# Optimization experiments

Measured on AMD Instinct MI355X. Metric: run time of the kernel, lower is better.

Reference implementation:

```python
import jax, jax.numpy as jnp
import numpy as np

EPS = 1e-5
NUM_SUBSET = 3

def conv1x1(x, w, b):
    # x: (N,C,T,V), w: (O,C), b: (O,)
    return jnp.einsum('nctv,oc->notv', x, w) + b[None, :, None, None]

def batchnorm(x, w, b):
    m = x.mean(axis=(0, 2, 3), keepdims=True)
    v = x.var(axis=(0, 2, 3), keepdims=True)
    return (x - m) * jax.lax.rsqrt(v + EPS) * w[None, :, None, None] + b[None, :, None, None]

def setup_inputs() -> dict:
    key = jax.random.key(0)
    ks = jax.random.split(key, 16)
    N, C, T, V, R, O, S = 32, 64, 256, 25, 8, 64, NUM_SUBSET
    sc = 0.05
    return {
        'x1': jax.random.normal(ks[0], (N, C, T, V), jnp.float32),
        'x2': jax.random.normal(ks[1], (N, C, T, V), jnp.float32),
        'PA': jax.random.normal(ks[2], (S, V, V), jnp.float32) * sc,
        'alpha': jnp.zeros((1,), jnp.float32),
        'c1w': jax.random.normal(ks[3], (S, R, C), jnp.float32) * sc,
        'c1b': jnp.zeros((S, R), jnp.float32),
        'c2w': jax.random.normal(ks[4], (S, R, C), jnp.float32) * sc,
        'c2b': jnp.zeros((S, R), jnp.float32),
        'c3w': jax.random.normal(ks[5], (S, O, C), jnp.float32) * sc,
        'c3b': jnp.zeros((S, O), jnp.float32),
        'c4w': jax.random.normal(ks[6], (S, O, C), jnp.float32) * sc,
        'c4b': jnp.zeros((S, O), jnp.float32),
        'c5w': jax.random.normal(ks[7], (S, O, R), jnp.float32) * sc,
        'c5b': jnp.zeros((S, O), jnp.float32),
        'c6w': jax.random.normal(ks[8], (S, O, R), jnp.float32) * sc,
        'c6b': jnp.zeros((S, O), jnp.float32),
        'bn1_w': jax.random.uniform(ks[9], (O,), jnp.float32),
        'bn1_b': jnp.zeros((O,), jnp.float32),
        'bn2_w': jax.random.uniform(ks[10], (O,), jnp.float32),
        'bn2_b': jnp.zeros((O,), jnp.float32),
    }

def reference(x1, x2, PA, alpha, c1w, c1b, c2w, c2b, c3w, c3b, c4w, c4b,
              c5w, c5b, c6w, c6b, bn1_w, bn1_b, bn2_w, bn2_b):
    y1 = y2 = None
    for i in range(NUM_SUBSET):
        r1 = conv1x1(x1, c1w[i], c1b[i]).mean(axis=2)  # (N,R,V)
        r2 = conv1x1(x2, c2w[i], c2b[i]).mean(axis=2)  # (N,R,V)
        x3 = conv1x1(x1, c3w[i], c3b[i])               # (N,O,T,V)
        x4 = conv1x1(x2, c4w[i], c4b[i])               # (N,O,T,V)
        rel = jnp.tanh(r1[:, :, :, None] - r2[:, :, None, :])  # (N,R,V,V)
        # NOTE: source passes self.alpha (scalar param) into the A2 slot,
        # so the `alpha` multiplier on conv5 defaults to 1.
        a1 = jnp.einsum('nruv,or->nouv', rel, c5w[i]) + c5b[i][None, :, None, None]
        a1 = a1 + PA[i][None, None, :, :]
        a2 = jnp.einsum('nruv,or->nouv', rel, c6w[i]) + c6b[i][None, :, None, None] + alpha
        z1 = jnp.einsum('ncuv,nctv->nctu', a1, x3)
        z2 = jnp.einsum('ncuv,nctv->nctu', a2, x4)
        y1 = z1 if y1 is None else y1 + z1
        y2 = z2 if y2 is None else y2 + z2
    # in_channels == out_channels -> residual down is identity
    y1 = jax.nn.relu(batchnorm(y1, bn1_w, bn1_b) + x1)
    y2 = jax.nn.relu(batchnorm(y2, bn2_w, bn2_b) + x2)
    return (y1, y2)
```

## Files before the change

kernel.cpp:

```cpp
#include <hip/hip_runtime.h>

typedef float  f32x4  __attribute__((ext_vector_type(4)));
typedef short  bf16x8 __attribute__((ext_vector_type(8)));
typedef short  s16x4  __attribute__((ext_vector_type(4)));

__device__ __forceinline__ unsigned short f2bf(float f) {
    unsigned int u = __float_as_uint(f);
    unsigned int r = (u + 0x7FFFu + ((u >> 16) & 1u)) >> 16;
    return (unsigned short)r;
}
__device__ __forceinline__ float bf2f(unsigned short h) {
    return __uint_as_float(((unsigned int)h) << 16);
}

__global__ __launch_bounds__(256) void kT_transpose(
    const float* __restrict__ x1, const float* __restrict__ x2,
    float* __restrict__ xm, unsigned short* __restrict__ xT)
{
    const int tc = blockIdx.x, n = blockIdx.y, p = blockIdx.z;
    const float* __restrict__ x = p ? x2 : x1;
    __shared__ unsigned short tile[64 * 225];
    const int tid = threadIdx.x;

    const size_t xb = (size_t)n * 409600 + (size_t)tc * 200;
    for (int k = 0; k < 13; k++) {
        const int idx = tid + k * 256;
        if (idx < 3200) {
            const int c = idx / 50, l = idx % 50;
            const f32x4 v = *(const f32x4*)(x + xb + (size_t)c * 6400 + l * 4);
            const int base = c * 225 + l * 4;
            tile[base + 0] = f2bf(v[0]);
            tile[base + 1] = f2bf(v[1]);
            tile[base + 2] = f2bf(v[2]);
            tile[base + 3] = f2bf(v[3]);
        }
    }
    __syncthreads();

    for (int k = 0; k < 7; k++) {
        const int idx = tid + k * 256;
        if (idx < 1600) {
            const int c = idx / 25, v = idx % 25;
            float s = 0.f;
            #pragma unroll
            for (int t = 0; t < 8; t++) s += bf2f(tile[c * 225 + t * 25 + v]);
            atomicAdd(&xm[((size_t)(p * 32 + n) * 64 + c) * 25 + v],
                      s * (1.0f / 256.0f));
        }
    }

    for (int k = 0; k < 7; k++) {
        const int idx = tid + k * 256;
        if (idx < 1600) {
            const int c8 = idx & 7, pos = idx >> 3;
            bf16x8 o;
            #pragma unroll
            for (int j = 0; j < 8; j++)
                o[j] = (short)tile[(c8 * 8 + j) * 225 + pos];
            *(bf16x8*)(xT + (((size_t)(p * 32 + n) * 6400 + tc * 200 + pos) * 64
                             + c8 * 8)) = o;
        }
    }
}

__global__ void k0b_pack(const float* __restrict__ c3w, const float* __restrict__ c4w,
                         unsigned short* __restrict__ awW)
{
    const int pi = blockIdx.x;
    const int p = pi / 3, i = pi % 3;
    const int tid = threadIdx.x;
    const int cg = tid >> 6, lane = tid & 63, q = lane >> 4, m = lane & 15;
    const float* w3 = p ? c4w : c3w;
    const float* wr = w3 + (size_t)(i * 64 + cg * 16 + m) * 64 + q * 8;
    const f32x4 w00 = *(const f32x4*)(wr);
    const f32x4 w01 = *(const f32x4*)(wr + 4);
    const f32x4 w10 = *(const f32x4*)(wr + 32);
    const f32x4 w11 = *(const f32x4*)(wr + 36);
    bf16x8 af0, af1;
    #pragma unroll
    for (int k = 0; k < 4; k++) {
        af0[k] = (short)f2bf(w00[k]); af0[k + 4] = (short)f2bf(w01[k]);
        af1[k] = (short)f2bf(w10[k]); af1[k + 4] = (short)f2bf(w11[k]);
    }
    unsigned short* o = awW + ((size_t)(pi * 4 + cg) * 64 + lane) * 16;
    *(bf16x8*)(o)     = af0;
    *(bf16x8*)(o + 8) = af1;
}

__global__ void k2_adj(const float* __restrict__ xm,
                       const float* __restrict__ PA, const float* __restrict__ alpha,
                       const float* __restrict__ c1w, const float* __restrict__ c1b,
                       const float* __restrict__ c2w, const float* __restrict__ c2b,
                       const float* __restrict__ c5w, const float* __restrict__ c5b,
                       const float* __restrict__ c6w, const float* __restrict__ c6b,
                       unsigned short* __restrict__ aw)
{
    const int b = blockIdx.x;
    const int i = b >> 6;
    const int n = (b >> 1) & 31;
    const int pp = b & 1;
    __shared__ float xml[3200];
    __shared__ float rl[400];
    __shared__ float rel[5000];
    const int tid = threadIdx.x;

    for (int idx = tid; idx < 3200; idx += 256) {
        const int p_ = idx / 1600, rest = idx % 1600;
        xml[idx] = xm[(size_t)(p_ * 32 + n) * 1600 + rest];
    }
    __syncthreads();

    for (int idx = tid; idx < 400; idx += 256) {
        const int which = idx / 200;
        const int rr = (idx % 200) / 25;
        const int v = idx % 25;
        const float* wv = (which ? c2w : c1w) + (i * 8 + rr) * 64;
        const float* xp = xml + which * 1600;
        float s = (which ? c2b : c1b)[i * 8 + rr];
        for (int c = 0; c < 64; c++) s += wv[c] * xp[c * 25 + v];
        rl[idx] = s;
    }
    __syncthreads();

    for (int idx = tid; idx < 5000; idx += 256) {
        const int r_ = idx / 625;
        const int rem = idx - r_ * 625;
        const int u = rem / 25;
        const int v = rem - u * 25;
        rel[idx] = tanhf(rl[r_ * 25 + u] - rl[200 + r_ * 25 + v]);
    }
    __syncthreads();

    const float al = alpha[0];
    {
        const int p_ = pp;
        const float* w5 = p_ ? c6w : c5w;
        const float* b5 = p_ ? c6b : c5b;
        for (int idx = tid; idx < 8192; idx += 256) {
            const int c = idx >> 7;
            const int ut = (idx >> 6) & 1;
            const int lane = idx & 63;
            const int u = ut * 16 + (lane & 15);
            const int qd = lane >> 4;
            bf16x8 outv;
            if (u < 25) {
                float wrow[8];
                #pragma unroll
                for (int r = 0; r < 8; r++) wrow[r] = w5[(i * 64 + c) * 8 + r];
                const float bias = b5[i * 64 + c];
                #pragma unroll
                for (int j = 0; j < 8; j++) {
                    const int v = qd * 8 + j;
                    float s = 0.f;
                    if (v < 25) {
                        s = bias + (p_ ? al : PA[i * 625 + u * 25 + v]);
                        #pragma unroll
                        for (int r = 0; r < 8; r++) s += rel[r * 625 + u * 25 + v] * wrow[r];
                    }
                    outv[j] = (short)f2bf(s);
                }
            } else {
                #pragma unroll
                for (int j = 0; j < 8; j++) outv[j] = 0;
            }
            *(bf16x8*)(aw + ((size_t)((p_ * 3 + i) * 32 + n) * 64 + c) * 1024
                          + ut * 512 + lane * 8) = outv;
        }
    }
}

__global__ __launch_bounds__(256, 4) void kF_main(
    const unsigned short* __restrict__ xT,
    const float* __restrict__ c3b, const float* __restrict__ c4b,
    const unsigned short* __restrict__ awW,
    const unsigned short* __restrict__ aw,
    unsigned short* __restrict__ z,
    float* __restrict__ ppart)
{
    const int bx = blockIdx.x;
    const int tc = bx & 15, cg = bx >> 4;
    const int n = blockIdx.y, p = blockIdx.z;
    __shared__ unsigned short X3s[16 * 512];
    const int tid = threadIdx.x, w = tid >> 6, lane = tid & 63;
    const int q = lane >> 4, m = lane & 15;

    {
        int* xi = (int*)X3s;
        #pragma unroll
        for (int k = 0; k < 16; k++) xi[tid + k * 256] = 0;
    }

    const float* __restrict__ b3 = p ? c4b : c3b;
    const size_t xTb = ((size_t)(p * 32 + n) * 6400 + (size_t)tc * 400) * 64;

    f32x4 acc[4][2];
    #pragma unroll
    for (int a = 0; a < 4; a++) {
        acc[a][0] = (f32x4){0.f, 0.f, 0.f, 0.f};
        acc[a][1] = (f32x4){0.f, 0.f, 0.f, 0.f};
    }

    __syncthreads();

    for (int i = 0; i < 3; i++) {
        const unsigned short* wp =
            awW + ((size_t)((p * 3 + i) * 4 + cg) * 64 + lane) * 16;
        const bf16x8 af0 = *(const bf16x8*)(wp);
        const bf16x8 af1 = *(const bf16x8*)(wp + 8);
        float bb[4];
        #pragma unroll
        for (int r = 0; r < 4; r++) bb[r] = b3[i * 64 + cg * 16 + q * 4 + r];

        for (int g = w; g < 25; g += 4) {
            const unsigned short* xp = xT + xTb + (size_t)(g * 16 + m) * 64 + q * 8;
            const bf16x8 xb0 = *(const bf16x8*)(xp);
            const bf16x8 xb1 = *(const bf16x8*)(xp + 32);
            f32x4 d = (f32x4){0.f, 0.f, 0.f, 0.f};
            d = __builtin_amdgcn_mfma_f32_16x16x32_bf16(af0, xb0, d, 0, 0, 0);
            d = __builtin_amdgcn_mfma_f32_16x16x32_bf16(af1, xb1, d, 0, 0, 0);
            const int pos = g * 16 + m;
            const int t = pos / 25, v = pos - t * 25;
            #pragma unroll
            for (int r = 0; r < 4; r++)
                X3s[(q * 4 + r) * 512 + t * 32 + v] = f2bf(d[r] + bb[r]);
        }
        __syncthreads();

        #pragma unroll
        for (int cl4 = 0; cl4 < 4; cl4++) {
            const int cl = w * 4 + cl4;
            const int c = cg * 16 + cl;
            const bf16x8 A = *(const bf16x8*)(X3s + cl * 512 + m * 32 + q * 8);
            const unsigned short* ab =
                aw + ((size_t)((p * 3 + i) * 32 + n) * 64 + c) * 1024 + lane * 8;
            const bf16x8 B0 = *(const bf16x8*)(ab);
            const bf16x8 B1 = *(const bf16x8*)(ab + 512);
            acc[cl4][0] = __builtin_amdgcn_mfma_f32_16x16x32_bf16(A, B0, acc[cl4][0], 0, 0, 0);
            acc[cl4][1] = __builtin_amdgcn_mfma_f32_16x16x32_bf16(A, B1, acc[cl4][1], 0, 0, 0);
        }
        __syncthreads();
    }

    #pragma unroll
    for (int cl4 = 0; cl4 < 4; cl4++) {
        float sum = 0.f, ssq = 0.f;
        #pragma unroll
        for (int r = 0; r < 4; r++) {
            const float v0 = acc[cl4][0][r];
            sum += v0; ssq += v0 * v0;
        }
        if (m < 9) {
            #pragma unroll
            for (int r = 0; r < 4; r++) {
                const float v1 = acc[cl4][1][r];
                sum += v1; ssq += v1 * v1;
            }
        }
        #pragma unroll
        for (int off = 32; off > 0; off >>= 1) {
            sum += __shfl_xor(sum, off, 64);
            ssq += __shfl_xor(ssq, off, 64);
        }
        const int c = cg * 16 + w * 4 + cl4;
        if (lane == 0) {
            float* pp = ppart + ((size_t)(p * 64 + c) * 512 + n * 16 + tc) * 2;
            pp[0] = sum; pp[1] = ssq;
        }
        #pragma unroll
        for (int ut = 0; ut < 2; ut++) {
            if (ut == 0 || m < 9) {
                #pragma unroll
                for (int r = 0; r < 4; r++)
                    X3s[w * 1600 + cl4 * 400 + (q * 4 + r) * 25 + ut * 16 + m] =
                        f2bf(acc[cl4][ut][r]);
            }
        }
    }
    for (int rd = 0; rd < 4; rd++) {
        const int idx = rd * 64 + lane;
        if (idx < 200) {
            const int cl4 = idx / 50, oct = idx % 50;
            const bf16x8 vz = *(const bf16x8*)(X3s + w * 1600 + cl4 * 400 + oct * 8);
            const int c = cg * 16 + w * 4 + cl4;
            *(bf16x8*)(z + ((size_t)((p * 32 + n) * 64 + c)) * 6400
                         + tc * 400 + oct * 8) = vz;
        }
    }
}

__global__ void k4_finalize(const float* __restrict__ ppart,
                            const float* __restrict__ bn1w, const float* __restrict__ bn1b,
                            const float* __restrict__ bn2w, const float* __restrict__ bn2b,
                            float* __restrict__ ss)
{
    const int b = blockIdx.x;
    const int t = threadIdx.x;
    const float* base = ppart + (size_t)b * 1024;
    float s = 0.f, qs = 0.f;
    #pragma unroll
    for (int k = 0; k < 8; k++) {
        const int idx = t + 64 * k;
        s  += base[idx * 2];
        qs += base[idx * 2 + 1];
    }
    #pragma unroll
    for (int off = 32; off > 0; off >>= 1) {
        s  += __shfl_xor(s,  off, 64);
        qs += __shfl_xor(qs, off, 64);
    }
    if (t == 0) {
        const int p = b >> 6, c = b & 63;
        const float cnt = 204800.f;
        const float mean = s / cnt;
        const float var  = qs / cnt - mean * mean;
        const float gw = p ? bn2w[c] : bn1w[c];
        const float gb = p ? bn2b[c] : bn1b[c];
        const float scale = gw * rsqrtf(var + 1e-5f);
        ss[b * 2]     = scale;
        ss[b * 2 + 1] = gb - mean * scale;
    }
}

__global__ void k5_apply(const float* __restrict__ x1, const float* __restrict__ x2,
                         const unsigned short* __restrict__ z, const float* __restrict__ ss,
                         float* __restrict__ out)
{
    const size_t g = (size_t)blockIdx.x * 256 + threadIdx.x;
    const size_t e = g * 4;
    const int p = (int)(e / 13107200u);
    const int c = (int)((e / 6400u) & 63);
    const float* xsrc = p ? x2 : x1;
    const f32x4 xv = *(const f32x4*)(xsrc + (e - (size_t)p * 13107200u));
    const s16x4 zv = *(const s16x4*)(const void*)(z + e);
    const float scale = ss[(p * 64 + c) * 2];
    const float shift = ss[(p * 64 + c) * 2 + 1];
    f32x4 o;
    #pragma unroll
    for (int k = 0; k < 4; k++) {
        const float zf = bf2f((unsigned short)zv[k]);
        const float y = zf * scale + shift + xv[k];
        o[k] = y > 0.f ? y : 0.f;
    }
    *(f32x4*)(out + e) = o;
}

extern "C" void kernel_launch(void* const* d_in, const int* in_sizes, int n_in,
                              void* d_out, int out_size, void* d_ws, size_t ws_size,
                              hipStream_t stream)
{
    (void)in_sizes; (void)n_in; (void)out_size; (void)ws_size;
    const float* x1   = (const float*)d_in[0];
    const float* x2   = (const float*)d_in[1];
    const float* PA   = (const float*)d_in[2];
    const float* alp  = (const float*)d_in[3];
    const float* c1w  = (const float*)d_in[4];
    const float* c1b  = (const float*)d_in[5];
    const float* c2w  = (const float*)d_in[6];
    const float* c2b  = (const float*)d_in[7];
    const float* c3w  = (const float*)d_in[8];
    const float* c3b  = (const float*)d_in[9];
    const float* c4w  = (const float*)d_in[10];
    const float* c4b  = (const float*)d_in[11];
    const float* c5w  = (const float*)d_in[12];
    const float* c5b  = (const float*)d_in[13];
    const float* c6w  = (const float*)d_in[14];
    const float* c6b  = (const float*)d_in[15];
    const float* bn1w = (const float*)d_in[16];
    const float* bn1b = (const float*)d_in[17];
    const float* bn2w = (const float*)d_in[18];
    const float* bn2b = (const float*)d_in[19];

    char* ws = (char*)d_ws;
    float*          xm    = (float*)(ws + 0);
    unsigned short* aw    = (unsigned short*)(ws + 409600);
    unsigned short* xT    = (unsigned short*)(ws + 25575424);
    unsigned short* zbuf  = (unsigned short*)(ws + 78004224);
    float*          ppart = (float*)(ws + 130433024);
    float*          ss    = (float*)(ws + 130957312);
    unsigned short* awW   = (unsigned short*)(ws + 130958336);

    hipMemsetAsync(xm, 0, 409600, stream);

    kT_transpose<<<dim3(32, 32, 2), 256, 0, stream>>>(x1, x2, xm, xT);
    k0b_pack<<<6, 256, 0, stream>>>(c3w, c4w, awW);
    k2_adj<<<192, 256, 0, stream>>>(xm, PA, alp, c1w, c1b, c2w, c2b,
                                    c5w, c5b, c6w, c6b, aw);
    kF_main<<<dim3(64, 32, 2), 256, 0, stream>>>(xT, c3b, c4b, awW, aw,
                                                 zbuf, ppart);
    k4_finalize<<<128, 64, 0, stream>>>(ppart, bn1w, bn1b, bn2w, bn2b, ss);
    k5_apply<<<25600, 256, 0, stream>>>(x1, x2, zbuf, ss, (float*)d_out);
}
```

Baseline: 421.1 us.

## Fuse weight pack into adjacency kernel, double-buffer LDS and prefetch in main kernel

The separate weight-pack launch is folded into extra blocks of the adjacency kernel, which removes one launch. The main kernel now holds its input tiles in registers across all three subsets, prefetches the adjacency B fragments before each stage, and double-buffers the LDS tile so one barrier per iteration can be dropped. Its 1D grid is remapped so that blocks sharing an (n,p) pair are spread across XCDs, and the occupancy hint drops from 4 to 3 blocks per CU. The apply kernel switches to 32-bit index math. Register pressure rises and LDS use doubles, which may reduce occupancy.

```diff
diff --git a/kernel.cpp b/kernel.cpp
--- a/kernel.cpp
+++ b/kernel.cpp
@@ -63,46 +63,47 @@
     }
 }
 
-__global__ void k0b_pack(const float* __restrict__ c3w, const float* __restrict__ c4w,
-                         unsigned short* __restrict__ awW)
-{
-    const int pi = blockIdx.x;
-    const int p = pi / 3, i = pi % 3;
-    const int tid = threadIdx.x;
-    const int cg = tid >> 6, lane = tid & 63, q = lane >> 4, m = lane & 15;
-    const float* w3 = p ? c4w : c3w;
-    const float* wr = w3 + (size_t)(i * 64 + cg * 16 + m) * 64 + q * 8;
-    const f32x4 w00 = *(const f32x4*)(wr);
-    const f32x4 w01 = *(const f32x4*)(wr + 4);
-    const f32x4 w10 = *(const f32x4*)(wr + 32);
-    const f32x4 w11 = *(const f32x4*)(wr + 36);
-    bf16x8 af0, af1;
-    #pragma unroll
-    for (int k = 0; k < 4; k++) {
-        af0[k] = (short)f2bf(w00[k]); af0[k + 4] = (short)f2bf(w01[k]);
-        af1[k] = (short)f2bf(w10[k]); af1[k + 4] = (short)f2bf(w11[k]);
-    }
-    unsigned short* o = awW + ((size_t)(pi * 4 + cg) * 64 + lane) * 16;
-    *(bf16x8*)(o)     = af0;
-    *(bf16x8*)(o + 8) = af1;
-}
-
 __global__ void k2_adj(const float* __restrict__ xm,
                        const float* __restrict__ PA, const float* __restrict__ alpha,
                        const float* __restrict__ c1w, const float* __restrict__ c1b,
                        const float* __restrict__ c2w, const float* __restrict__ c2b,
                        const float* __restrict__ c5w, const float* __restrict__ c5b,
                        const float* __restrict__ c6w, const float* __restrict__ c6b,
-                       unsigned short* __restrict__ aw)
+                       unsigned short* __restrict__ aw,
+                       const float* __restrict__ c3w, const float* __restrict__ c4w,
+                       unsigned short* __restrict__ awW)
 {
     const int b = blockIdx.x;
+    const int tid = threadIdx.x;
+
+    if (b >= 192) {
+        const int pi = b - 192;
+        const int p = pi / 3, i = pi % 3;
+        const int cg = tid >> 6, lane = tid & 63, q = lane >> 4, m = lane & 15;
+        const float* w3 = p ? c4w : c3w;
+        const float* wr = w3 + (size_t)(i * 64 + cg * 16 + m) * 64 + q * 8;
+        const f32x4 w00 = *(const f32x4*)(wr);
+        const f32x4 w01 = *(const f32x4*)(wr + 4);
+        const f32x4 w10 = *(const f32x4*)(wr + 32);
+        const f32x4 w11 = *(const f32x4*)(wr + 36);
+        bf16x8 af0, af1;
+        #pragma unroll
+        for (int k = 0; k < 4; k++) {
+            af0[k] = (short)f2bf(w00[k]); af0[k + 4] = (short)f2bf(w01[k]);
+            af1[k] = (short)f2bf(w10[k]); af1[k + 4] = (short)f2bf(w11[k]);
+        }
+        unsigned short* o = awW + ((size_t)(pi * 4 + cg) * 64 + lane) * 16;
+        *(bf16x8*)(o)     = af0;
+        *(bf16x8*)(o + 8) = af1;
+        return;
+    }
+
     const int i = b >> 6;
     const int n = (b >> 1) & 31;
     const int pp = b & 1;
     __shared__ float xml[3200];
     __shared__ float rl[400];
     __shared__ float rel[5000];
-    const int tid = threadIdx.x;
 
     for (int idx = tid; idx < 3200; idx += 256) {
         const int p_ = idx / 1600, rest = idx % 1600;
@@ -169,7 +170,7 @@
     }
 }
 
-__global__ __launch_bounds__(256, 4) void kF_main(
+__global__ __launch_bounds__(256, 3) void kF_main(
     const unsigned short* __restrict__ xT,
     const float* __restrict__ c3b, const float* __restrict__ c4b,
     const unsigned short* __restrict__ awW,
@@ -177,21 +178,36 @@
     unsigned short* __restrict__ z,
     float* __restrict__ ppart)
 {
-    const int bx = blockIdx.x;
-    const int tc = bx & 15, cg = bx >> 4;
-    const int n = blockIdx.y, p = blockIdx.z;
-    __shared__ unsigned short X3s[16 * 512];
+    const int flat = blockIdx.x;
+    const int lidx = flat >> 3;
+    const int grp  = (flat & 7) * 8 + (lidx >> 6);
+    const int within = lidx & 63;
+    const int tc = within & 15, cg = within >> 4;
+    const int n = grp & 31, p = grp >> 5;
+
+    __shared__ unsigned short X3s[2][16 * 512];
     const int tid = threadIdx.x, w = tid >> 6, lane = tid & 63;
     const int q = lane >> 4, m = lane & 15;
 
     {
-        int* xi = (int*)X3s;
-        #pragma unroll
-        for (int k = 0; k < 16; k++) xi[tid + k * 256] = 0;
+        int* xi = (int*)&X3s[0][0];
+        #pragma unroll
+        for (int k = 0; k < 32; k++) xi[tid + k * 256] = 0;
     }
 
     const float* __restrict__ b3 = p ? c4b : c3b;
     const size_t xTb = ((size_t)(p * 32 + n) * 6400 + (size_t)tc * 400) * 64;
+
+    bf16x8 xr0[7], xr1[7];
+    #pragma unroll
+    for (int k = 0; k < 7; k++) {
+        const int g = w + 4 * k;
+        if (g < 25) {
+            const unsigned short* xp = xT + xTb + (size_t)(g * 16 + m) * 64 + q * 8;
+            xr0[k] = *(const bf16x8*)(xp);
+            xr1[k] = *(const bf16x8*)(xp + 32);
+        }
+    }
 
     f32x4 acc[4][2];
     #pragma unroll
@@ -203,6 +219,16 @@
     __syncthreads();
 
     for (int i = 0; i < 3; i++) {
+        bf16x8 B0[4], B1[4];
+        #pragma unroll
+        for (int cl4 = 0; cl4 < 4; cl4++) {
+            const int c = cg * 16 + w * 4 + cl4;
+            const unsigned short* ab =
+                aw + ((size_t)((p * 3 + i) * 32 + n) * 64 + c) * 1024 + lane * 8;
+            B0[cl4] = *(const bf16x8*)(ab);
+            B1[cl4] = *(const bf16x8*)(ab + 512);
+        }
+
         const unsigned short* wp =
             awW + ((size_t)((p * 3 + i) * 4 + cg) * 64 + lane) * 16;
         const bf16x8 af0 = *(const bf16x8*)(wp);
@@ -211,36 +237,34 @@
         #pragma unroll
         for (int r = 0; r < 4; r++) bb[r] = b3[i * 64 + cg * 16 + q * 4 + r];
 
-        for (int g = w; g < 25; g += 4) {
-            const unsigned short* xp = xT + xTb + (size_t)(g * 16 + m) * 64 + q * 8;
-            const bf16x8 xb0 = *(const bf16x8*)(xp);
-            const bf16x8 xb1 = *(const bf16x8*)(xp + 32);
-            f32x4 d = (f32x4){0.f, 0.f, 0.f, 0.f};
-            d = __builtin_amdgcn_mfma_f32_16x16x32_bf16(af0, xb0, d, 0, 0, 0);
-            d = __builtin_amdgcn_mfma_f32_16x16x32_bf16(af1, xb1, d, 0, 0, 0);
-            const int pos = g * 16 + m;
-            const int t = pos / 25, v = pos - t * 25;
-            #pragma unroll
-            for (int r = 0; r < 4; r++)
-                X3s[(q * 4 + r) * 512 + t * 32 + v] = f2bf(d[r] + bb[r]);
+        unsigned short* Xb = &X3s[i & 1][0];
+        #pragma unroll
+        for (int k = 0; k < 7; k++) {
+            const int g = w + 4 * k;
+            if (g < 25) {
+                f32x4 d = (f32x4){0.f, 0.f, 0.f, 0.f};
+                d = __builtin_amdgcn_mfma_f32_16x16x32_bf16(af0, xr0[k], d, 0, 0, 0);
+                d = __builtin_amdgcn_mfma_f32_16x16x32_bf16(af1, xr1[k], d, 0, 0, 0);
+                const int pos = g * 16 + m;
+                const int t = pos / 25, v = pos - t * 25;
+                #pragma unroll
+                for (int r = 0; r < 4; r++)
+                    Xb[(q * 4 + r) * 512 + t * 32 + v] = f2bf(d[r] + bb[r]);
+            }
         }
         __syncthreads();
 
         #pragma unroll
         for (int cl4 = 0; cl4 < 4; cl4++) {
             const int cl = w * 4 + cl4;
-            const int c = cg * 16 + cl;
-            const bf16x8 A = *(const bf16x8*)(X3s + cl * 512 + m * 32 + q * 8);
-            const unsigned short* ab =
-                aw + ((size_t)((p * 3 + i) * 32 + n) * 64 + c) * 1024 + lane * 8;
-            const bf16x8 B0 = *(const bf16x8*)(ab);
-            const bf16x8 B1 = *(const bf16x8*)(ab + 512);
-            acc[cl4][0] = __builtin_amdgcn_mfma_f32_16x16x32_bf16(A, B0, acc[cl4][0], 0, 0, 0);
-            acc[cl4][1] = __builtin_amdgcn_mfma_f32_16x16x32_bf16(A, B1, acc[cl4][1], 0, 0, 0);
-        }
-        __syncthreads();
-    }
-
+            const bf16x8 A = *(const bf16x8*)(Xb + cl * 512 + m * 32 + q * 8);
+            acc[cl4][0] = __builtin_amdgcn_mfma_f32_16x16x32_bf16(A, B0[cl4], acc[cl4][0], 0, 0, 0);
+            acc[cl4][1] = __builtin_amdgcn_mfma_f32_16x16x32_bf16(A, B1[cl4], acc[cl4][1], 0, 0, 0);
+        }
+    }
+    __syncthreads();
+
+    unsigned short* stg = &X3s[0][0];
     #pragma unroll
     for (int cl4 = 0; cl4 < 4; cl4++) {
         float sum = 0.f, ssq = 0.f;
@@ -271,7 +295,7 @@
             if (ut == 0 || m < 9) {
                 #pragma unroll
                 for (int r = 0; r < 4; r++)
-                    X3s[w * 1600 + cl4 * 400 + (q * 4 + r) * 25 + ut * 16 + m] =
+                    stg[w * 1600 + cl4 * 400 + (q * 4 + r) * 25 + ut * 16 + m] =
                         f2bf(acc[cl4][ut][r]);
             }
         }
@@ -280,7 +304,7 @@
         const int idx = rd * 64 + lane;
         if (idx < 200) {
             const int cl4 = idx / 50, oct = idx % 50;
-            const bf16x8 vz = *(const bf16x8*)(X3s + w * 1600 + cl4 * 400 + oct * 8);
+            const bf16x8 vz = *(const bf16x8*)(stg + w * 1600 + cl4 * 400 + oct * 8);
             const int c = cg * 16 + w * 4 + cl4;
             *(bf16x8*)(z + ((size_t)((p * 32 + n) * 64 + c)) * 6400
                          + tc * 400 + oct * 8) = vz;
@@ -321,16 +345,17 @@
     }
 }
 
-__global__ void k5_apply(const float* __restrict__ x1, const float* __restrict__ x2,
-                         const unsigned short* __restrict__ z, const float* __restrict__ ss,
-                         float* __restrict__ out)
-{
-    const size_t g = (size_t)blockIdx.x * 256 + threadIdx.x;
-    const size_t e = g * 4;
-    const int p = (int)(e / 13107200u);
-    const int c = (int)((e / 6400u) & 63);
+__global__ __launch_bounds__(256) void k5_apply(
+    const float* __restrict__ x1, const float* __restrict__ x2,
+    const unsigned short* __restrict__ z, const float* __restrict__ ss,
+    float* __restrict__ out)
+{
+    const unsigned int g = blockIdx.x * 256u + threadIdx.x;
+    const unsigned int e = g * 4u;
+    const int p = (e >= 13107200u) ? 1 : 0;
+    const unsigned int c = (e / 6400u) & 63u;
     const float* xsrc = p ? x2 : x1;
-    const f32x4 xv = *(const f32x4*)(xsrc + (e - (size_t)p * 13107200u));
+    const f32x4 xv = *(const f32x4*)(xsrc + (e - (unsigned int)p * 13107200u));
     const s16x4 zv = *(const s16x4*)(const void*)(z + e);
     const float scale = ss[(p * 64 + c) * 2];
     const float shift = ss[(p * 64 + c) * 2 + 1];
@@ -382,11 +407,10 @@
     hipMemsetAsync(xm, 0, 409600, stream);
 
     kT_transpose<<<dim3(32, 32, 2), 256, 0, stream>>>(x1, x2, xm, xT);
-    k0b_pack<<<6, 256, 0, stream>>>(c3w, c4w, awW);
-    k2_adj<<<192, 256, 0, stream>>>(xm, PA, alp, c1w, c1b, c2w, c2b,
-                                    c5w, c5b, c6w, c6b, aw);
-    kF_main<<<dim3(64, 32, 2), 256, 0, stream>>>(xT, c3b, c4b, awW, aw,
-                                                 zbuf, ppart);
+    k2_adj<<<198, 256, 0, stream>>>(xm, PA, alp, c1w, c1b, c2w, c2b,
+                                    c5w, c5b, c6w, c6b, aw, c3w, c4w, awW);
+    kF_main<<<dim3(4096), 256, 0, stream>>>(xT, c3b, c4b, awW, aw,
+                                            zbuf, ppart);
     k4_finalize<<<128, 64, 0, stream>>>(ppart, bn1w, bn1b, bn2w, bn2b, ss);
     k5_apply<<<25600, 256, 0, stream>>>(x1, x2, zbuf, ss, (float*)d_out);
 }
```

New measurement: 373.8 us. 1.13x faster.
